# Optimization experiments

Measured on AMD Instinct MI355X. Metric: run time of the kernel, lower is better.

Reference implementation:

```python
import jax, jax.numpy as jnp
import numpy as np

BLOCK_Q = 64
BLOCK_KV = 64
TOPK_RATIO = 0.125


def setup_inputs() -> dict:
    key = jax.random.key(0)
    k1, k2, k3 = jax.random.split(key, 3)
    B, H, L, D = 1, 16, 8192, 64
    q = jax.random.normal(k1, (B, H, L, D), dtype=jnp.float32)
    k = jax.random.normal(k2, (B, H, L, D), dtype=jnp.float32)
    v = jax.random.normal(k3, (B, H, L, D), dtype=jnp.float32)
    return {"q": q, "k": k, "v": v}


def _sparse_lut(q, k):
    # get_sparse_map: block mean-pool q and mean-centered k, score blocks, top-k key blocks
    B, H, L, D = q.shape
    Mb, Nb = L // BLOCK_Q, L // BLOCK_KV
    q_pool = q.reshape(B, H, Mb, BLOCK_Q, D).mean(axis=3)          # [B,H,Mb,D]
    smooth_k = k - k.mean(axis=-2, keepdims=True)
    k_pool = smooth_k.reshape(B, H, Nb, BLOCK_KV, D).mean(axis=3)  # [B,H,Nb,D]
    pred = jnp.einsum('bhmd,bhnd->bhmn', q_pool, k_pool)           # [B,H,Mb,Nb]
    topk = int(TOPK_RATIO * Nb)
    _, lut = jax.lax.top_k(pred, topk)                             # [B,H,Mb,topk]
    return lut


def reference(q, k, v):
    B, H, L, D = q.shape
    Mb, Nb = L // BLOCK_Q, L // BLOCK_KV
    lut = _sparse_lut(q, k)                                        # [B,H,Mb,T] int32
    T = lut.shape[-1]
    sm_scale = D ** -0.5

    kb = k.reshape(B, H, Nb, BLOCK_KV, D)
    vb = v.reshape(B, H, Nb, BLOCK_KV, D)
    bi = jnp.arange(B)[:, None, None, None]
    hi = jnp.arange(H)[None, :, None, None]
    # gather selected KV blocks per query block: [B,H,Mb,T,BLOCK_KV,D]
    k_sel = kb[bi, hi, lut].reshape(B, H, Mb, T * BLOCK_KV, D)
    v_sel = vb[bi, hi, lut].reshape(B, H, Mb, T * BLOCK_KV, D)

    qb = q.reshape(B, H, Mb, BLOCK_Q, D)
    s = jnp.einsum('bhmqd,bhmkd->bhmqk', qb, k_sel) * sm_scale     # [B,H,Mb,BQ,T*BKV]
    p = jax.nn.softmax(s, axis=-1)
    o = jnp.einsum('bhmqk,bhmkd->bhmqd', p, v_sel)
    return o.reshape(B, H, L, D)
```

## Files before the change

### kernel.cpp

```cpp
#include <hip/hip_runtime.h>
#include <hip/hip_bf16.h>


#define H_  16
#define L_  8192
#define D_  64
#define MB_ 128
#define NB_ 128
#define TK_ 16
#define ST_ 72
#define PST 72

typedef __bf16 bf16x8 __attribute__((ext_vector_type(8)));
typedef float  f32x4  __attribute__((ext_vector_type(4)));
typedef unsigned short u16x8 __attribute__((ext_vector_type(8)));

union BFU { __hip_bfloat16 h; unsigned short u; };

static __device__ inline unsigned short f2bfu(float f) {
  BFU c; c.h = __float2bfloat16(f); return c.u;
}

__device__ unsigned short g_qb[(size_t)H_ * L_ * D_];
__device__ unsigned short g_kb[(size_t)H_ * L_ * D_];
__device__ unsigned short g_vt[(size_t)H_ * D_ * L_];
__device__ float g_qpool[H_ * NB_ * 64];
__device__ float g_kpool[H_ * NB_ * 64];
__device__ int   g_lut[H_ * MB_ * TK_];

static __device__ inline void cvt8_2(const float4& f0, const float4& f1,
                                     unsigned short* dst) {
  u16x8 s;
  s[0] = f2bfu(f0.x); s[1] = f2bfu(f0.y); s[2] = f2bfu(f0.z); s[3] = f2bfu(f0.w);
  s[4] = f2bfu(f1.x); s[5] = f2bfu(f1.y); s[6] = f2bfu(f1.z); s[7] = f2bfu(f1.w);
  *(u16x8*)dst = s;
}

static __device__ inline void cvt8_2s(const float4& f0, const float4& f1,
                                      unsigned short* dst, float sc) {
  u16x8 s;
  s[0] = f2bfu(f0.x * sc); s[1] = f2bfu(f0.y * sc);
  s[2] = f2bfu(f0.z * sc); s[3] = f2bfu(f0.w * sc);
  s[4] = f2bfu(f1.x * sc); s[5] = f2bfu(f1.y * sc);
  s[6] = f2bfu(f1.z * sc); s[7] = f2bfu(f1.w * sc);
  *(u16x8*)dst = s;
}

__global__ __launch_bounds__(256)
void fusedpool_kernel(const float* __restrict__ q,
                      const float* __restrict__ k,
                      const float* __restrict__ v) {
  __shared__ float qt[64 * 64];
  __shared__ float kt[64 * 64];
  __shared__ __align__(16) unsigned short vt_s[64 * ST_];
  __shared__ float pq[4][64], pk[4][64];

  const int b = blockIdx.x;
  const int h = b >> 7, n = b & 127;
  const int t = threadIdx.x;
  const int r = t >> 2, c = (t & 3) * 16;
  const size_t base = (size_t)b * 4096 + r * 64 + c;
  const float cs = 0.18033688011112042f;

  float4 qf0 = *(const float4*)(q + base),      qf1 = *(const float4*)(q + base + 4);
  float4 qf2 = *(const float4*)(q + base + 8),  qf3 = *(const float4*)(q + base + 12);
  float4 kf0 = *(const float4*)(k + base),      kf1 = *(const float4*)(k + base + 4);
  float4 kf2 = *(const float4*)(k + base + 8),  kf3 = *(const float4*)(k + base + 12);
  float4 vf0 = *(const float4*)(v + base),      vf1 = *(const float4*)(v + base + 4);
  float4 vf2 = *(const float4*)(v + base + 8),  vf3 = *(const float4*)(v + base + 12);

  cvt8_2s(qf0, qf1, g_qb + base, cs);  cvt8_2s(qf2, qf3, g_qb + base + 8, cs);
  cvt8_2(kf0, kf1, g_kb + base);       cvt8_2(kf2, kf3, g_kb + base + 8);
  cvt8_2(vf0, vf1, vt_s + r * ST_ + c);
  cvt8_2(vf2, vf3, vt_s + r * ST_ + c + 8);

  *(float4*)(qt + r * 64 + c)      = qf0; *(float4*)(qt + r * 64 + c + 4)  = qf1;
  *(float4*)(qt + r * 64 + c + 8)  = qf2; *(float4*)(qt + r * 64 + c + 12) = qf3;
  *(float4*)(kt + r * 64 + c)      = kf0; *(float4*)(kt + r * 64 + c + 4)  = kf1;
  *(float4*)(kt + r * 64 + c + 8)  = kf2; *(float4*)(kt + r * 64 + c + 12) = kf3;
  __syncthreads();

  const int col = t & 63, g = t >> 6;
  float sq = 0.f, sk = 0.f;
  for (int rr = g * 16; rr < g * 16 + 16; ++rr) {
    sq += qt[rr * 64 + col];
    sk += kt[rr * 64 + col];
  }
  pq[g][col] = sq; pk[g][col] = sk;

  u16x8 va, vb;
  #pragma unroll
  for (int i = 0; i < 8; ++i) va[i] = vt_s[(c + i) * ST_ + r];
  #pragma unroll
  for (int i = 0; i < 8; ++i) vb[i] = vt_s[(c + 8 + i) * ST_ + r];
  const size_t vo = ((size_t)h * 64 + r) * (size_t)L_ + (size_t)n * 64 + c;
  *(u16x8*)(g_vt + vo)     = va;
  *(u16x8*)(g_vt + vo + 8) = vb;

  __syncthreads();
  if (t < 64) {
    g_qpool[b * 64 + t] = (pq[0][t] + pq[1][t] + pq[2][t] + pq[3][t]) * (1.f / 64.f);
    g_kpool[b * 64 + t] = (pk[0][t] + pk[1][t] + pk[2][t] + pk[3][t]) * (1.f / 64.f);
  }
}


__global__ void topk_kernel() {
  const int b = blockIdx.x;
  const int h = b >> 7;
  const int lane = threadIdx.x;
  const float4* qrow = (const float4*)(g_qpool + b * 64);
  const float4* k0 = (const float4*)(g_kpool + (h * NB_ + lane) * 64);
  const float4* k1 = (const float4*)(g_kpool + (h * NB_ + lane + 64) * 64);
  float v0 = 0.f, v1 = 0.f;
  for (int i = 0; i < 16; ++i) {
    float4 qv = qrow[i];
    float4 a = k0[i];
    float4 c = k1[i];
    v0 += qv.x * a.x + qv.y * a.y + qv.z * a.z + qv.w * a.w;
    v1 += qv.x * c.x + qv.y * c.y + qv.z * c.z + qv.w * c.w;
  }
  for (int t = 0; t < TK_; ++t) {
    float bv; int bi;
    if (v0 >= v1) { bv = v0; bi = lane; } else { bv = v1; bi = lane + 64; }
    for (int mask = 1; mask < 64; mask <<= 1) {
      float ov = __shfl_xor(bv, mask, 64);
      int   oi = __shfl_xor(bi, mask, 64);
      if (ov > bv || (ov == bv && oi < bi)) { bv = ov; bi = oi; }
    }
    if (lane == 0) g_lut[b * TK_ + t] = bi;
    if (bi == lane) v0 = -3.0e38f;
    else if (bi == lane + 64) v1 = -3.0e38f;
  }
}

__global__ __launch_bounds__(256, 4)
void attn_kernel(float* __restrict__ out) {
  __shared__ __align__(16) unsigned short Ks[2][64 * ST_];
  __shared__ __align__(16) unsigned short Vt[2][64 * ST_];
  __shared__ __align__(16) unsigned short Pw[4][16 * PST];

  const int blk = blockIdx.x;
  const int h = blk & 15, m = blk >> 4;
  const int t = threadIdx.x;
  const int w = t >> 6;
  const int lane = t & 63;
  const int l16 = lane & 15, quad = lane >> 4;
  const int srow = t >> 3, scol = (t & 7) * 8;
  const int vd = t >> 2, vc = (t & 3) * 16;

  const unsigned short* qg = g_qb + ((size_t)h * L_ + (size_t)m * 64) * D_;
  const unsigned short* qrow = qg + (16 * w + l16) * 64 + quad * 8;
  const bf16x8 aq0 = *(const bf16x8*)(qrow);
  const bf16x8 aq1 = *(const bf16x8*)(qrow + 32);

  f32x4 o[4];
  #pragma unroll
  for (int n4 = 0; n4 < 4; ++n4) o[n4] = (f32x4){0.f, 0.f, 0.f, 0.f};
  float lsum = 0.f;

  const int* my_lut = g_lut + (h * MB_ + m) * TK_;
  const unsigned short* kh = g_kb + (size_t)h * L_ * D_;
  const unsigned short* vg = g_vt + (size_t)h * D_ * L_;

  int kb = __builtin_amdgcn_readfirstlane(my_lut[0]);
  u16x8 kx0 = *(const u16x8*)(kh + kb * 4096 + t * 8);
  u16x8 kx1 = *(const u16x8*)(kh + kb * 4096 + 2048 + t * 8);
  u16x8 vx0 = *(const u16x8*)(vg + (size_t)vd * L_ + kb * 64 + vc);
  u16x8 vx1 = *(const u16x8*)(vg + (size_t)vd * L_ + kb * 64 + vc + 8);

  for (int j = 0; j < TK_; ++j) {
    const int buf = j & 1;
    *(u16x8*)(Ks[buf] + srow * ST_ + scol)        = kx0;
    *(u16x8*)(Ks[buf] + (32 + srow) * ST_ + scol) = kx1;
    *(u16x8*)(Vt[buf] + vd * ST_ + vc)     = vx0;
    *(u16x8*)(Vt[buf] + vd * ST_ + vc + 8) = vx1;

    if (j + 1 < TK_) {
      const int kbn = __builtin_amdgcn_readfirstlane(my_lut[j + 1]);
      kx0 = *(const u16x8*)(kh + kbn * 4096 + t * 8);
      kx1 = *(const u16x8*)(kh + kbn * 4096 + 2048 + t * 8);
      vx0 = *(const u16x8*)(vg + (size_t)vd * L_ + kbn * 64 + vc);
      vx1 = *(const u16x8*)(vg + (size_t)vd * L_ + kbn * 64 + vc + 8);
    }

    __syncthreads();

    f32x4 acc[4];
    __builtin_amdgcn_s_setprio(1);
    #pragma unroll
    for (int n4 = 0; n4 < 4; ++n4) {
      bf16x8 a0 = *(const bf16x8*)&Ks[buf][(n4 * 16 + l16) * ST_ + quad * 8];
      bf16x8 a1 = *(const bf16x8*)&Ks[buf][(n4 * 16 + l16) * ST_ + 32 + quad * 8];
      f32x4 z = (f32x4){0.f, 0.f, 0.f, 0.f};
      z = __builtin_amdgcn_mfma_f32_16x16x32_bf16(a0, aq0, z, 0, 0, 0);
      z = __builtin_amdgcn_mfma_f32_16x16x32_bf16(a1, aq1, z, 0, 0, 0);
      acc[n4] = z;
    }
    __builtin_amdgcn_s_setprio(0);

    unsigned short* pw = &Pw[w][0];
    #pragma unroll
    for (int n4 = 0; n4 < 4; ++n4) {
      const float p0 = exp2f(acc[n4][0]), p1 = exp2f(acc[n4][1]);
      const float p2 = exp2f(acc[n4][2]), p3 = exp2f(acc[n4][3]);
      lsum += (p0 + p1) + (p2 + p3);
      unsigned int d0, d1;
      asm("v_cvt_pk_bf16_f32 %0, %1, %2" : "=v"(d0) : "v"(p0), "v"(p1));
      asm("v_cvt_pk_bf16_f32 %0, %1, %2" : "=v"(d1) : "v"(p2), "v"(p3));
      uint2 dd; dd.x = d0; dd.y = d1;
      *(uint2*)&pw[l16 * PST + n4 * 16 + quad * 4] = dd;
    }

    asm volatile("s_waitcnt lgkmcnt(0)" ::: "memory");
    __builtin_amdgcn_sched_barrier(0);

    const bf16x8 pa0 = *(const bf16x8*)&pw[l16 * PST + quad * 8];
    const bf16x8 pa1 = *(const bf16x8*)&pw[l16 * PST + 32 + quad * 8];

    __builtin_amdgcn_s_setprio(1);
    #pragma unroll
    for (int n4 = 0; n4 < 4; ++n4) {
      bf16x8 v0f = *(const bf16x8*)&Vt[buf][(n4 * 16 + l16) * ST_ + quad * 8];
      bf16x8 v1f = *(const bf16x8*)&Vt[buf][(n4 * 16 + l16) * ST_ + 32 + quad * 8];
      o[n4] = __builtin_amdgcn_mfma_f32_16x16x32_bf16(pa0, v0f, o[n4], 0, 0, 0);
      o[n4] = __builtin_amdgcn_mfma_f32_16x16x32_bf16(pa1, v1f, o[n4], 0, 0, 0);
    }
    __builtin_amdgcn_s_setprio(0);
  }

  float rs = lsum;
  rs += __shfl_xor(rs, 16, 64);
  rs += __shfl_xor(rs, 32, 64);
  const float rinv = 1.0f / rs;
  float ri[4];
  #pragma unroll
  for (int r = 0; r < 4; ++r) ri[r] = __shfl(rinv, quad * 4 + r, 64);

  const size_t obase = ((size_t)h * L_ + (size_t)m * 64) * D_;
  #pragma unroll
  for (int n4 = 0; n4 < 4; ++n4) {
    #pragma unroll
    for (int r = 0; r < 4; ++r) {
      const int qrow_o = 16 * w + quad * 4 + r;
      out[obase + (size_t)qrow_o * 64 + n4 * 16 + l16] = o[n4][r] * ri[r];
    }
  }
}

extern "C" void kernel_launch(void* const* d_in, const int* in_sizes, int n_in,
                              void* d_out, int out_size, void* d_ws, size_t ws_size,
                              hipStream_t stream) {
  const float* q = (const float*)d_in[0];
  const float* k = (const float*)d_in[1];
  const float* v = (const float*)d_in[2];
  float* out = (float*)d_out;

  fusedpool_kernel<<<H_ * NB_, 256, 0, stream>>>(q, k, v);
  topk_kernel<<<H_ * MB_, 64, 0, stream>>>();
  attn_kernel<<<H_ * MB_, 256, 0, stream>>>(out);
}
```

Measured before the change: 236.3 us.

## Split attention work across warps by KV rows, keeping K/V in registers without LDS

The attention kernel now has each warp own 16 of the 64 key rows of every selected KV block for all 64 queries, instead of owning 16 query rows and sharing the whole block. K and V fragments are loaded straight from global memory into registers with double buffering, which removes the LDS staging, the P round-trip through shared memory and the per-iteration __syncthreads. The PV product uses 16x16x16 MFMAs with P taken directly from registers. The cost is a 64-element accumulator per thread and a cross-warp reduction of partial outputs and row sums through LDS at the end. Launch bounds drop to 3 blocks per SM to make room for the extra registers, and the V loads become strided 8-byte gathers.

```diff
diff --git a/kernel.cpp b/kernel.cpp
--- a/kernel.cpp
+++ b/kernel.cpp
@@ -9,9 +9,10 @@
 #define NB_ 128
 #define TK_ 16
 #define ST_ 72
-#define PST 72
 
 typedef __bf16 bf16x8 __attribute__((ext_vector_type(8)));
+typedef __bf16 bf16x4 __attribute__((ext_vector_type(4)));
+typedef short  s16x4  __attribute__((ext_vector_type(4)));
 typedef float  f32x4  __attribute__((ext_vector_type(4)));
 typedef unsigned short u16x8 __attribute__((ext_vector_type(8)));
 
@@ -19,6 +20,19 @@
 
 static __device__ inline unsigned short f2bfu(float f) {
   BFU c; c.h = __float2bfloat16(f); return c.u;
+}
+
+static __device__ inline f32x4 mfma16(bf16x4 a, bf16x4 b, f32x4 c) {
+#if __has_builtin(__builtin_amdgcn_mfma_f32_16x16x16bf16_1k)
+  return __builtin_amdgcn_mfma_f32_16x16x16bf16_1k(
+      __builtin_bit_cast(s16x4, a), __builtin_bit_cast(s16x4, b), c, 0, 0, 0);
+#elif __has_builtin(__builtin_amdgcn_mfma_f32_16x16x16_bf16)
+  return __builtin_amdgcn_mfma_f32_16x16x16_bf16(a, b, c, 0, 0, 0);
+#else
+  f32x4 d = c;
+  asm("v_mfma_f32_16x16x16_bf16 %0, %1, %2, %0" : "+v"(d) : "v"(a), "v"(b));
+  return d;
+#endif
 }
 
 __device__ unsigned short g_qb[(size_t)H_ * L_ * D_];
@@ -134,11 +148,10 @@
   }
 }
 
-__global__ __launch_bounds__(256, 4)
+__global__ __launch_bounds__(256, 3)
 void attn_kernel(float* __restrict__ out) {
-  __shared__ __align__(16) unsigned short Ks[2][64 * ST_];
-  __shared__ __align__(16) unsigned short Vt[2][64 * ST_];
-  __shared__ __align__(16) unsigned short Pw[4][16 * PST];
+  __shared__ float LDSo[4][16][65];
+  __shared__ float LDSr[4][64];
 
   const int blk = blockIdx.x;
   const int h = blk & 15, m = blk >> 4;
@@ -146,105 +159,127 @@
   const int w = t >> 6;
   const int lane = t & 63;
   const int l16 = lane & 15, quad = lane >> 4;
-  const int srow = t >> 3, scol = (t & 7) * 8;
-  const int vd = t >> 2, vc = (t & 3) * 16;
 
   const unsigned short* qg = g_qb + ((size_t)h * L_ + (size_t)m * 64) * D_;
-  const unsigned short* qrow = qg + (16 * w + l16) * 64 + quad * 8;
-  const bf16x8 aq0 = *(const bf16x8*)(qrow);
-  const bf16x8 aq1 = *(const bf16x8*)(qrow + 32);
-
-  f32x4 o[4];
-  #pragma unroll
-  for (int n4 = 0; n4 < 4; ++n4) o[n4] = (f32x4){0.f, 0.f, 0.f, 0.f};
-  float lsum = 0.f;
+  bf16x8 qb0[4], qb1[4];
+  #pragma unroll
+  for (int g = 0; g < 4; ++g) {
+    const unsigned short* qp = qg + (16 * g + l16) * 64 + quad * 8;
+    qb0[g] = *(const bf16x8*)(qp);
+    qb1[g] = *(const bf16x8*)(qp + 32);
+  }
+
+  f32x4 o[4][4];
+  #pragma unroll
+  for (int n4 = 0; n4 < 4; ++n4)
+    #pragma unroll
+    for (int g = 0; g < 4; ++g) o[n4][g] = (f32x4){0.f, 0.f, 0.f, 0.f};
+  float lsum[4] = {0.f, 0.f, 0.f, 0.f};
 
   const int* my_lut = g_lut + (h * MB_ + m) * TK_;
   const unsigned short* kh = g_kb + (size_t)h * L_ * D_;
   const unsigned short* vg = g_vt + (size_t)h * D_ * L_;
-
-  int kb = __builtin_amdgcn_readfirstlane(my_lut[0]);
-  u16x8 kx0 = *(const u16x8*)(kh + kb * 4096 + t * 8);
-  u16x8 kx1 = *(const u16x8*)(kh + kb * 4096 + 2048 + t * 8);
-  u16x8 vx0 = *(const u16x8*)(vg + (size_t)vd * L_ + kb * 64 + vc);
-  u16x8 vx1 = *(const u16x8*)(vg + (size_t)vd * L_ + kb * 64 + vc + 8);
-
+  const int krow = (16 * w + l16) * 64 + quad * 8;
+  const int vcol = 16 * w + quad * 4;
+
+  bf16x8 ka0[2], ka1[2];
+  bf16x4 va[2][4];
+
+  {
+    const int kb0 = __builtin_amdgcn_readfirstlane(my_lut[0]);
+    const unsigned short* kbp = kh + (size_t)kb0 * 4096 + krow;
+    ka0[0] = *(const bf16x8*)(kbp);
+    ka1[0] = *(const bf16x8*)(kbp + 32);
+    const unsigned short* vbp = vg + (size_t)kb0 * 64 + vcol;
+    #pragma unroll
+    for (int n4 = 0; n4 < 4; ++n4)
+      va[0][n4] = *(const bf16x4*)(vbp + (size_t)(16 * n4 + l16) * L_);
+  }
+
+  #pragma unroll
   for (int j = 0; j < TK_; ++j) {
-    const int buf = j & 1;
-    *(u16x8*)(Ks[buf] + srow * ST_ + scol)        = kx0;
-    *(u16x8*)(Ks[buf] + (32 + srow) * ST_ + scol) = kx1;
-    *(u16x8*)(Vt[buf] + vd * ST_ + vc)     = vx0;
-    *(u16x8*)(Vt[buf] + vd * ST_ + vc + 8) = vx1;
-
+    const int cb = j & 1, nb = cb ^ 1;
     if (j + 1 < TK_) {
       const int kbn = __builtin_amdgcn_readfirstlane(my_lut[j + 1]);
-      kx0 = *(const u16x8*)(kh + kbn * 4096 + t * 8);
-      kx1 = *(const u16x8*)(kh + kbn * 4096 + 2048 + t * 8);
-      vx0 = *(const u16x8*)(vg + (size_t)vd * L_ + kbn * 64 + vc);
-      vx1 = *(const u16x8*)(vg + (size_t)vd * L_ + kbn * 64 + vc + 8);
-    }
-
-    __syncthreads();
+      const unsigned short* kbp = kh + (size_t)kbn * 4096 + krow;
+      ka0[nb] = *(const bf16x8*)(kbp);
+      ka1[nb] = *(const bf16x8*)(kbp + 32);
+      const unsigned short* vbp = vg + (size_t)kbn * 64 + vcol;
+      #pragma unroll
+      for (int n4 = 0; n4 < 4; ++n4)
+        va[nb][n4] = *(const bf16x4*)(vbp + (size_t)(16 * n4 + l16) * L_);
+    }
 
     f32x4 acc[4];
     __builtin_amdgcn_s_setprio(1);
     #pragma unroll
-    for (int n4 = 0; n4 < 4; ++n4) {
-      bf16x8 a0 = *(const bf16x8*)&Ks[buf][(n4 * 16 + l16) * ST_ + quad * 8];
-      bf16x8 a1 = *(const bf16x8*)&Ks[buf][(n4 * 16 + l16) * ST_ + 32 + quad * 8];
+    for (int g = 0; g < 4; ++g) {
       f32x4 z = (f32x4){0.f, 0.f, 0.f, 0.f};
-      z = __builtin_amdgcn_mfma_f32_16x16x32_bf16(a0, aq0, z, 0, 0, 0);
-      z = __builtin_amdgcn_mfma_f32_16x16x32_bf16(a1, aq1, z, 0, 0, 0);
-      acc[n4] = z;
+      z = __builtin_amdgcn_mfma_f32_16x16x32_bf16(ka0[cb], qb0[g], z, 0, 0, 0);
+      z = __builtin_amdgcn_mfma_f32_16x16x32_bf16(ka1[cb], qb1[g], z, 0, 0, 0);
+      acc[g] = z;
     }
     __builtin_amdgcn_s_setprio(0);
 
-    unsigned short* pw = &Pw[w][0];
-    #pragma unroll
-    for (int n4 = 0; n4 < 4; ++n4) {
-      const float p0 = exp2f(acc[n4][0]), p1 = exp2f(acc[n4][1]);
-      const float p2 = exp2f(acc[n4][2]), p3 = exp2f(acc[n4][3]);
-      lsum += (p0 + p1) + (p2 + p3);
+    bf16x4 pb[4];
+    #pragma unroll
+    for (int g = 0; g < 4; ++g) {
+      const float p0 = exp2f(acc[g][0]), p1 = exp2f(acc[g][1]);
+      const float p2 = exp2f(acc[g][2]), p3 = exp2f(acc[g][3]);
+      lsum[g] += (p0 + p1) + (p2 + p3);
       unsigned int d0, d1;
       asm("v_cvt_pk_bf16_f32 %0, %1, %2" : "=v"(d0) : "v"(p0), "v"(p1));
       asm("v_cvt_pk_bf16_f32 %0, %1, %2" : "=v"(d1) : "v"(p2), "v"(p3));
       uint2 dd; dd.x = d0; dd.y = d1;
-      *(uint2*)&pw[l16 * PST + n4 * 16 + quad * 4] = dd;
-    }
-
-    asm volatile("s_waitcnt lgkmcnt(0)" ::: "memory");
-    __builtin_amdgcn_sched_barrier(0);
-
-    const bf16x8 pa0 = *(const bf16x8*)&pw[l16 * PST + quad * 8];
-    const bf16x8 pa1 = *(const bf16x8*)&pw[l16 * PST + 32 + quad * 8];
+      pb[g] = __builtin_bit_cast(bf16x4, dd);
+    }
 
     __builtin_amdgcn_s_setprio(1);
     #pragma unroll
-    for (int n4 = 0; n4 < 4; ++n4) {
-      bf16x8 v0f = *(const bf16x8*)&Vt[buf][(n4 * 16 + l16) * ST_ + quad * 8];
-      bf16x8 v1f = *(const bf16x8*)&Vt[buf][(n4 * 16 + l16) * ST_ + 32 + quad * 8];
-      o[n4] = __builtin_amdgcn_mfma_f32_16x16x32_bf16(pa0, v0f, o[n4], 0, 0, 0);
-      o[n4] = __builtin_amdgcn_mfma_f32_16x16x32_bf16(pa1, v1f, o[n4], 0, 0, 0);
-    }
+    for (int n4 = 0; n4 < 4; ++n4)
+      #pragma unroll
+      for (int g = 0; g < 4; ++g)
+        o[n4][g] = mfma16(va[cb][n4], pb[g], o[n4][g]);
     __builtin_amdgcn_s_setprio(0);
   }
 
-  float rs = lsum;
-  rs += __shfl_xor(rs, 16, 64);
-  rs += __shfl_xor(rs, 32, 64);
-  const float rinv = 1.0f / rs;
-  float ri[4];
-  #pragma unroll
-  for (int r = 0; r < 4; ++r) ri[r] = __shfl(rinv, quad * 4 + r, 64);
+  #pragma unroll
+  for (int g = 0; g < 4; ++g) {
+    float rs = lsum[g];
+    rs += __shfl_xor(rs, 16, 64);
+    rs += __shfl_xor(rs, 32, 64);
+    lsum[g] = rs;
+  }
+  if (quad == 0) {
+    #pragma unroll
+    for (int g = 0; g < 4; ++g) LDSr[w][16 * g + l16] = lsum[g];
+  }
+  __syncthreads();
+
+  const int dr = t & 15, q0 = (t >> 4) * 4;
+  float rinv[4];
+  #pragma unroll
+  for (int qq = 0; qq < 4; ++qq)
+    rinv[qq] = 1.0f / (LDSr[0][q0 + qq] + LDSr[1][q0 + qq] +
+                       LDSr[2][q0 + qq] + LDSr[3][q0 + qq]);
 
   const size_t obase = ((size_t)h * L_ + (size_t)m * 64) * D_;
   #pragma unroll
   for (int n4 = 0; n4 < 4; ++n4) {
     #pragma unroll
-    for (int r = 0; r < 4; ++r) {
-      const int qrow_o = 16 * w + quad * 4 + r;
-      out[obase + (size_t)qrow_o * 64 + n4 * 16 + l16] = o[n4][r] * ri[r];
-    }
+    for (int g = 0; g < 4; ++g)
+      #pragma unroll
+      for (int r = 0; r < 4; ++r)
+        LDSo[w][quad * 4 + r][16 * g + l16] = o[n4][g][r];
+    __syncthreads();
+    #pragma unroll
+    for (int qq = 0; qq < 4; ++qq) {
+      const int qv = q0 + qq;
+      const float s = LDSo[0][dr][qv] + LDSo[1][dr][qv] +
+                      LDSo[2][dr][qv] + LDSo[3][dr][qv];
+      out[obase + (size_t)qv * 64 + n4 * 16 + dr] = s * rinv[qq];
+    }
+    __syncthreads();
   }
 }
 
```

Measured after the change: 266.4 us. 1.13x slower.
